# Performance work log

Hardware: AMD Instinct MI355X
Metric: run time of the kernel (lower is better)

The kernel has to match this reference:

```python
import jax, jax.numpy as jnp
from jax import lax
import numpy as np

B, S, T = 32, 512, 64
IN, H, L, HC, OUT = 512, 512, 2, 4, 512

def setup_inputs() -> dict:
    key = jax.random.key(0)
    ks = jax.random.split(key, 12)
    def w(k, shape, fan_in):
        return (jax.random.normal(k, shape, jnp.float32) / np.float32(np.sqrt(fan_in)))
    lstm_in0 = IN + HC * H
    return {
        "inputs": jax.random.normal(ks[0], (B, T, IN), jnp.float32),
        "lengths": jax.random.randint(ks[1], (B,), 1, S + 1),
        "final_hiddens": jax.random.normal(ks[2], (L, B, H), jnp.float32),
        "hiddens": jax.random.normal(ks[3], (B, S, H), jnp.float32),
        "max_output_len": T,
        "max_seq_len": S,
        "Wa1": w(ks[4], (H, 2 * H), 2 * H), "ba1": jnp.zeros((H,), jnp.float32),
        "Wa2": w(ks[5], (HC, H), H), "ba2": jnp.zeros((HC,), jnp.float32),
        "W_ih0": w(ks[6], (4 * H, lstm_in0), lstm_in0), "W_hh0": w(ks[7], (4 * H, H), H),
        "b_ih0": jnp.zeros((4 * H,), jnp.float32), "b_hh0": jnp.zeros((4 * H,), jnp.float32),
        "W_ih1": w(ks[8], (4 * H, H), H), "W_hh1": w(ks[9], (4 * H, H), H),
        "b_ih1": jnp.zeros((4 * H,), jnp.float32), "b_hh1": jnp.zeros((4 * H,), jnp.float32),
        "Wo1": w(ks[10], (H, (1 + HC) * H), (1 + HC) * H), "bo1": jnp.zeros((H,), jnp.float32),
        "Wo2": w(ks[11], (OUT, H), H), "bo2": jnp.zeros((OUT,), jnp.float32),
    }

def _lstm_cell(x, h, c, W_ih, W_hh, b_ih, b_hh):
    # PyTorch LSTM gate order: i, f, g, o
    g = x @ W_ih.T + b_ih + h @ W_hh.T + b_hh
    i, f, gg, o = jnp.split(g, 4, axis=-1)
    c_new = jax.nn.sigmoid(f) * c + jax.nn.sigmoid(i) * jnp.tanh(gg)
    h_new = jax.nn.sigmoid(o) * jnp.tanh(c_new)
    return h_new, c_new

def reference(inputs, lengths, final_hiddens, hiddens, max_output_len, max_seq_len,
              Wa1, ba1, Wa2, ba2, W_ih0, W_hh0, b_ih0, b_hh0,
              W_ih1, W_hh1, b_ih1, b_hh1, Wo1, bo1, Wo2, bo2):
    batch = inputs.shape[0]
    # r_mask[b, s] = 1 if s < lengths[b] else 0  -> [B, S, 1]
    r_mask = (jnp.arange(max_seq_len)[None, :] < lengths[:, None]).astype(hiddens.dtype)[..., None]

    def step(carry, x_t):
        h, c = carry  # each [L, B, H]
        last = h[-1]  # [B, H]
        dup = last[:, None, :] * r_mask  # [B, S, H]
        a = jax.nn.relu(jnp.concatenate([dup, hiddens], axis=2) @ Wa1.T + ba1)  # [B,S,H]
        a = jax.nn.relu(a @ Wa2.T + ba2)  # [B,S,HC]
        a = jax.nn.softmax(a, axis=1)  # softmax over seq dim (unmasked, as in source)
        c_vecs = jnp.einsum('bsk,bsh->bkh', a, hiddens).reshape(batch, -1)  # [B, HC*H]
        x = jnp.concatenate([x_t, c_vecs], axis=1)  # [B, IN + HC*H]
        h0, c0 = _lstm_cell(x, h[0], c[0], W_ih0, W_hh0, b_ih0, b_hh0)
        h1, c1 = _lstm_cell(h0, h[1], c[1], W_ih1, W_hh1, b_ih1, b_hh1)
        out = jnp.tanh(jax.nn.relu(jnp.concatenate([h1, c_vecs], axis=1) @ Wo1.T + bo1) @ Wo2.T + bo2)
        return (jnp.stack([h0, h1]), jnp.stack([c0, c1])), out

    c_init = jnp.zeros_like(final_hiddens)
    _, outs = lax.scan(step, (final_hiddens, c_init), jnp.swapaxes(inputs, 0, 1))  # [T,B,OUT]
    return jnp.swapaxes(outs, 0, 1)  # [B, T, OUT]
```

## Files before the change

kernel.cpp:

```cpp
#include <hip/hip_runtime.h>
#include <cmath>


typedef unsigned short ushort;
typedef unsigned int uint;
typedef __attribute__((ext_vector_type(8))) short bf16x8;
typedef __attribute__((ext_vector_type(4))) float f32x4;

__device__ __forceinline__ float sigmoidf_(float x) { return 1.f / (1.f + __expf(-x)); }
__device__ __forceinline__ float bf2f(ushort u) {
  union { uint i; float f; } x; x.i = ((uint)u) << 16; return x.f;
}
__device__ __forceinline__ ushort f2bf(float f) {
  union { float f; uint i; } x; x.f = f;
  return (ushort)((x.i + 0x7FFFu + ((x.i >> 16) & 1u)) >> 16);
}
__device__ __forceinline__ float wave_sum(float v) {
#pragma unroll
  for (int m = 1; m < 64; m <<= 1) v += __shfl_xor(v, m, 64);
  return v;
}
__device__ __forceinline__ float wave_max(float v) {
#pragma unroll
  for (int m = 1; m < 64; m <<= 1) v = fmaxf(v, __shfl_xor(v, m, 64));
  return v;
}

__global__ void __launch_bounds__(256) k_init(const float* __restrict__ fh,
                                              ushort* h0b0, ushort* h1b0,
                                              float* c0, float* c1) {
  int i = blockIdx.x * 256 + threadIdx.x;
  h0b0[i] = f2bf(fh[i]);
  h1b0[i] = f2bf(fh[16384 + i]);
  c0[i] = 0.f; c1[i] = 0.f;
}

__global__ void __launch_bounds__(256) k_prep(const float* __restrict__ hid,
                                              ushort* __restrict__ hbf) {
  size_t i0 = ((size_t)blockIdx.x * 256 + threadIdx.x) * 8;
  float4 f0 = *(const float4*)&hid[i0];
  float4 f1 = *(const float4*)&hid[i0 + 4];
  uint4 o;
  o.x = (uint)f2bf(f0.x) | ((uint)f2bf(f0.y) << 16);
  o.y = (uint)f2bf(f0.z) | ((uint)f2bf(f0.w) << 16);
  o.z = (uint)f2bf(f1.x) | ((uint)f2bf(f1.y) << 16);
  o.w = (uint)f2bf(f1.z) | ((uint)f2bf(f1.w) << 16);
  *(uint4*)&hbf[i0] = o;
}

__global__ void __launch_bounds__(256) k_inprep(const float* __restrict__ inputs,
                                                ushort* __restrict__ inb) {
  size_t idx4 = ((size_t)blockIdx.x * 256 + threadIdx.x) * 4;
  int m = (int)(idx4 >> 9), k = (int)(idx4 & 511);
  int b = m & 31, tt = m >> 5;
  float4 v = *(const float4*)&inputs[((size_t)b * 64 + tt) * 512 + k];
  ushort4 o; o.x = f2bf(v.x); o.y = f2bf(v.y); o.z = f2bf(v.z); o.w = f2bf(v.w);
  *(ushort4*)&inb[(size_t)m * 512 + k] = o;
}

__global__ void __launch_bounds__(256) k_wcvt(const float* __restrict__ W1, int ld1,
                                              const float* __restrict__ W2, int ld2,
                                              int split, int K,
                                              ushort* __restrict__ dst) {
  size_t idx = ((size_t)blockIdx.x * 256 + threadIdx.x) * 4;
  int j = (int)(idx / K), k = (int)(idx % K);
  const float* src = (k < split) ? (W1 + (size_t)j * ld1 + k)
                                 : (W2 + (size_t)j * ld2 + (k - split));
  float4 v = *(const float4*)src;
  ushort4 o; o.x = f2bf(v.x); o.y = f2bf(v.y); o.z = f2bf(v.z); o.w = f2bf(v.w);
  *(ushort4*)&dst[idx] = o;
}

__global__ void __launch_bounds__(256) k_hidproj(const float* __restrict__ hid,
                                                 const float* __restrict__ Wa1,
                                                 ushort* __restrict__ hpT) {
  __shared__ float As[64][33];
  __shared__ float Bs[64][33];
  int tid = threadIdx.x;
  int r0 = blockIdx.x * 64;
  int n0 = blockIdx.y * 64;
  int b = r0 >> 9, sb = r0 & 511;
  int tm = (tid >> 4) << 2, tn = (tid & 15) << 2;
  int lr = tid >> 2, lk = (tid & 3) << 3;
  float acc[4][4] = {};
  for (int k0 = 0; k0 < 512; k0 += 32) {
    float4 a0 = *(const float4*)&hid[(size_t)(r0 + lr) * 512 + k0 + lk];
    float4 a1 = *(const float4*)&hid[(size_t)(r0 + lr) * 512 + k0 + lk + 4];
    float4 b0 = *(const float4*)&Wa1[(size_t)(n0 + lr) * 1024 + 512 + k0 + lk];
    float4 b1 = *(const float4*)&Wa1[(size_t)(n0 + lr) * 1024 + 512 + k0 + lk + 4];
    __syncthreads();
    As[lr][lk+0]=a0.x; As[lr][lk+1]=a0.y; As[lr][lk+2]=a0.z; As[lr][lk+3]=a0.w;
    As[lr][lk+4]=a1.x; As[lr][lk+5]=a1.y; As[lr][lk+6]=a1.z; As[lr][lk+7]=a1.w;
    Bs[lr][lk+0]=b0.x; Bs[lr][lk+1]=b0.y; Bs[lr][lk+2]=b0.z; Bs[lr][lk+3]=b0.w;
    Bs[lr][lk+4]=b1.x; Bs[lr][lk+5]=b1.y; Bs[lr][lk+6]=b1.z; Bs[lr][lk+7]=b1.w;
    __syncthreads();
#pragma unroll 8
    for (int kk = 0; kk < 32; kk++) {
      float av[4], bv[4];
#pragma unroll
      for (int i = 0; i < 4; i++) av[i] = As[tm + i][kk];
#pragma unroll
      for (int j = 0; j < 4; j++) bv[j] = Bs[tn + j][kk];
#pragma unroll
      for (int i = 0; i < 4; i++)
#pragma unroll
        for (int j = 0; j < 4; j++) acc[i][j] += av[i] * bv[j];
    }
  }
#pragma unroll
  for (int j = 0; j < 4; j++) {
    ushort4 o;
    o.x = f2bf(acc[0][j]); o.y = f2bf(acc[1][j]);
    o.z = f2bf(acc[2][j]); o.w = f2bf(acc[3][j]);
    *(ushort4*)&hpT[((size_t)b * 512 + n0 + tn + j) * 512 + sb + tm] = o;
  }
}

__global__ void __launch_bounds__(512) k_scst(const ushort* __restrict__ hpT,
                                              const float* __restrict__ ba1,
                                              const float* __restrict__ Wa2,
                                              float* __restrict__ scoresP) {
  int bid = blockIdx.x, tid = threadIdx.x;
  int b = bid >> 3, kdq = bid & 7, kd0 = kdq << 6, s = tid;
  float a0 = 0.f, a1 = 0.f, a2 = 0.f, a3 = 0.f;
  const ushort* hpr = hpT + ((size_t)b * 512 + kd0) * 512 + s;
#pragma unroll 4
  for (int i = 0; i < 64; i++) {
    int kd = kd0 + i;
    float a = fmaxf(bf2f(hpr[(size_t)i * 512]) + ba1[kd], 0.f);
    a0 += Wa2[kd] * a;
    a1 += Wa2[512 + kd] * a;
    a2 += Wa2[1024 + kd] * a;
    a3 += Wa2[1536 + kd] * a;
  }
  float* dst = scoresP + ((size_t)(kdq * 32 + b) * 4) * 512 + s;
  dst[0] = a0; dst[512] = a1; dst[1024] = a2; dst[1536] = a3;
}

__global__ void __launch_bounds__(512) k_sum0(const float* __restrict__ scoresP,
                                              const float* __restrict__ ba2,
                                              float* __restrict__ scores0) {
  int idx = blockIdx.x * 512 + threadIdx.x;
  int b = idx >> 11, k = (idx >> 9) & 3, s = idx & 511;
  float v = ba2[k];
#pragma unroll
  for (int q = 0; q < 8; q++) v += scoresP[((size_t)(q * 32 + b) * 4 + k) * 512 + s];
  scores0[idx] = fmaxf(v, 0.f);
}

__global__ void __launch_bounds__(512) k_stat0(const float* __restrict__ scores0,
                                               const int* __restrict__ lengths,
                                               float* __restrict__ m0v,
                                               float* __restrict__ statZ,
                                               float* __restrict__ P0) {
  __shared__ float st[32], st2[32];
  int b = blockIdx.x, tid = threadIdx.x, lane = tid & 63, w = tid >> 6;
  int s = tid, len = lengths[b];
  bool stat = s >= len;
  float v[4], m0[4];
#pragma unroll
  for (int k = 0; k < 4; k++) v[k] = scores0[((size_t)b * 4 + k) * 512 + s];
#pragma unroll
  for (int k = 0; k < 4; k++) {
    float mk = wave_max(stat ? v[k] : -1e30f);
    if (lane == 0) st[w * 4 + k] = mk;
  }
  __syncthreads();
#pragma unroll
  for (int k = 0; k < 4; k++) {
    float m = st[k];
#pragma unroll
    for (int w2 = 1; w2 < 8; w2++) m = fmaxf(m, st[w2 * 4 + k]);
    m0[k] = m;
  }
  float e[4];
#pragma unroll
  for (int k = 0; k < 4; k++) {
    e[k] = stat ? __expf(v[k] - m0[k]) : 0.f;
    float sk = wave_sum(e[k]);
    if (lane == 0) st2[w * 4 + k] = sk;
  }
  __syncthreads();
#pragma unroll
  for (int k = 0; k < 4; k++) {
    P0[((size_t)b * 4 + k) * 512 + s] = e[k];
  }
  if (tid == 0) {
#pragma unroll
    for (int k = 0; k < 4; k++) {
      float z = 0.f;
#pragma unroll
      for (int w2 = 0; w2 < 8; w2++) z += st2[w2 * 4 + k];
      m0v[b * 4 + k] = m0[k];
      statZ[b * 4 + k] = z;
    }
  }
}

__global__ void __launch_bounds__(512) k_statvec(const float* __restrict__ P0,
                                                 const ushort* __restrict__ hbf,
                                                 const int* __restrict__ lengths,
                                                 float* __restrict__ statvec) {
  __shared__ float P[4 * 512];
  __shared__ float red2[8 * 256];
  int bid = blockIdx.x, tid = threadIdx.x;
  int b = bid >> 3, hs = bid & 7;
#pragma unroll
  for (int k = 0; k < 4; k++) P[k * 512 + tid] = P0[((size_t)b * 4 + k) * 512 + tid];
  __syncthreads();
  int h = tid & 63, cch = tid >> 6;
  int c0 = lengths[b] >> 6;
  float a0 = 0.f, a1 = 0.f, a2 = 0.f, a3 = 0.f;
  if (cch >= c0) {
    const ushort* hb = hbf + ((size_t)(b * 512 + (cch << 6)) * 512) + (hs << 6) + h;
#pragma unroll 4
    for (int si = 0; si < 64; si++) {
      float hv = bf2f(hb[(size_t)si * 512]);
      int ps = (cch << 6) + si;
      a0 += P[ps] * hv;
      a1 += P[512 + ps] * hv;
      a2 += P[1024 + ps] * hv;
      a3 += P[1536 + ps] * hv;
    }
  }
  red2[(cch << 8) + h] = a0;
  red2[(cch << 8) + 64 + h] = a1;
  red2[(cch << 8) + 128 + h] = a2;
  red2[(cch << 8) + 192 + h] = a3;
  __syncthreads();
  if (tid < 256) {
    int k = tid >> 6, hh = tid & 63;
    float acc = 0.f;
#pragma unroll
    for (int c = 0; c < 8; c++) acc += red2[(c << 8) + (k << 6) + hh];
    statvec[((size_t)b * 4 + k) * 512 + (hs << 6) + hh] = acc;
  }
}

__device__ __forceinline__ void mfma_slice(
    const ushort* __restrict__ W, int ldW, int jrow0, int jstride,
    const ushort* __restrict__ xA, int ldA, int xsplit,
    const ushort* __restrict__ xB, int ldB, int coff,
    int klo, int khi, float* __restrict__ redrow) {
  const int l = threadIdx.x & 63;
  const int r16 = l & 15, koff = (l >> 4) * 8;
  const int j = jrow0 + (r16 & 3) + (r16 >> 2) * jstride;
  const ushort* wrow = W + (size_t)j * ldW + koff;
  const ushort* a0A = xA + (size_t)r16 * ldA + koff;
  const ushort* a1A = xA + (size_t)(16 + r16) * ldA + koff;
  const ushort* a0B = xB + (size_t)r16 * ldB + koff;
  const ushort* a1B = xB + (size_t)(16 + r16) * ldB + koff;
  f32x4 acc0 = {0.f, 0.f, 0.f, 0.f}, acc1 = {0.f, 0.f, 0.f, 0.f};
#pragma unroll 4
  for (int k0 = klo; k0 < khi; k0 += 32) {
    bf16x8 av0, av1;
    if (k0 < xsplit) {
      av0 = *(const bf16x8*)(a0A + k0);
      av1 = *(const bf16x8*)(a1A + k0);
    } else {
      av0 = *(const bf16x8*)(a0B + (k0 - coff));
      av1 = *(const bf16x8*)(a1B + (k0 - coff));
    }
    bf16x8 wv = *(const bf16x8*)(wrow + k0);
    acc0 = __builtin_amdgcn_mfma_f32_16x16x32_bf16(av0, wv, acc0, 0, 0, 0);
    acc1 = __builtin_amdgcn_mfma_f32_16x16x32_bf16(av1, wv, acc1, 0, 0, 0);
  }
  const int brow = (l >> 4) << 2;
#pragma unroll
  for (int r = 0; r < 4; r++) {
    redrow[r16 * 33 + brow + r] = acc0[r];
    redrow[r16 * 33 + 16 + brow + r] = acc1[r];
  }
}

__global__ void __launch_bounds__(256) k_gin0(const ushort* __restrict__ Wg0b,
                                              const ushort* __restrict__ inb,
                                              float* __restrict__ gi0) {
  __shared__ float red[4 * 528];
  int tid = threadIdx.x, w = tid >> 6;
  int j0 = blockIdx.x * 16, m0 = blockIdx.y * 32;
  mfma_slice(Wg0b, 3072, j0, 4, inb + (size_t)m0 * 512, 512, 1 << 30,
             inb + (size_t)m0 * 512, 512, 0, w * 128, w * 128 + 128,
             red + w * 528);
  __syncthreads();
#pragma unroll
  for (int e = 0; e < 2; e++) {
    int idx = tid + e * 256;
    int j = idx >> 5, b = idx & 31;
    float v = 0.f;
#pragma unroll
    for (int ww = 0; ww < 4; ww++) v += red[ww * 528 + j * 33 + b];
    gi0[(size_t)(m0 + b) * 2048 + j0 + j] = v;
  }
}

__global__ void __launch_bounds__(512) k_scq(
    const ushort* __restrict__ Wq, const ushort* __restrict__ Wo1,
    const ushort* __restrict__ h1cur, const ushort* __restrict__ xb,
    const float* __restrict__ bo1, ushort* __restrict__ o1bf,
    const ushort* __restrict__ hpT, const float* __restrict__ ba1,
    const float* __restrict__ Wa2, const int* __restrict__ lengths,
    float* __restrict__ scoresP, int t) {
  __shared__ float red[8 * 528];
  __shared__ float qs[64];
  int bid = blockIdx.x, tid = threadIdx.x, w = tid >> 6, lane = tid & 63;
  if (bid < 32) {
    if (t < 1) return;
    mfma_slice(Wo1, 2560, bid * 16, 4, h1cur, 512, 512, xb, 2048, 512,
               w * 320, w * 320 + 320, red + w * 528);
    __syncthreads();
    int j = tid & 15, b = tid >> 4;
    float v = 0.f;
#pragma unroll
    for (int ww = 0; ww < 8; ww++) v += red[ww * 528 + j * 33 + b];
    int jj = bid * 16 + j;
    o1bf[b * 512 + jj] = f2bf(fmaxf(v + bo1[jj], 0.f));
  } else {
    if (t >= 64) return;
    int r = bid - 32;
    int b = r >> 3, kdq = r & 7, kd0 = kdq << 6;
    {
      bf16x8 hv8 = *(const bf16x8*)(h1cur + b * 512 + lane * 8);
      float hf[8];
#pragma unroll
      for (int e2 = 0; e2 < 8; e2++) hf[e2] = bf2f(((ushort*)&hv8)[e2]);
#pragma unroll
      for (int rr = 0; rr < 8; rr++) {
        int row = kd0 + w * 8 + rr;
        bf16x8 wv8 = *(const bf16x8*)(Wq + (size_t)row * 512 + lane * 8);
        float acc = 0.f;
#pragma unroll
        for (int e2 = 0; e2 < 8; e2++) acc += hf[e2] * bf2f(((ushort*)&wv8)[e2]);
        acc = wave_sum(acc);
        if (lane == 0) qs[w * 8 + rr] = acc;
      }
    }
    __syncthreads();
    int s = tid, len = lengths[b];
    if ((tid & ~63) >= len) return;
    float m = (s < len) ? 1.f : 0.f;
    float a0 = 0.f, a1 = 0.f, a2 = 0.f, a3 = 0.f;
    const ushort* hpr = hpT + ((size_t)b * 512 + kd0) * 512 + s;
#pragma unroll 4
    for (int i = 0; i < 64; i++) {
      int kd = kd0 + i;
      float hv = bf2f(hpr[(size_t)i * 512]);
      float a = fmaxf(hv + ba1[kd] + m * qs[i], 0.f);
      a0 += Wa2[kd] * a;
      a1 += Wa2[512 + kd] * a;
      a2 += Wa2[1024 + kd] * a;
      a3 += Wa2[1536 + kd] * a;
    }
    float* dst = scoresP + ((size_t)(kdq * 32 + b) * 4) * 512 + s;
    dst[0] = a0; dst[512] = a1; dst[1024] = a2; dst[1536] = a3;
  }
}

__global__ void __launch_bounds__(512) k_ctxout(
    const float* __restrict__ scoresP, const float* __restrict__ ba2,
    const int* __restrict__ lengths, const ushort* __restrict__ hbf,
    const float* __restrict__ m0v, const float* __restrict__ statZ,
    const float* __restrict__ statvec, ushort* __restrict__ xb,
    const ushort* __restrict__ Wo2, const ushort* __restrict__ o1bf,
    const float* __restrict__ bo2, float* __restrict__ outp, int t) {
  __shared__ float red[8 * 528];
  __shared__ float P[4 * 512];
  __shared__ float red2[8 * 256];
  __shared__ float st[32], st2[32];
  int bid = blockIdx.x, tid = threadIdx.x;
  if (bid < 32) {
    if (t < 1) return;
    int w = tid >> 6;
    mfma_slice(Wo2, 512, bid * 16, 4, o1bf, 512, 1 << 30, o1bf, 512, 0,
               w * 64, w * 64 + 64, red + w * 528);
    __syncthreads();
    int j = tid & 15, b = tid >> 4;
    float v = 0.f;
#pragma unroll
    for (int ww = 0; ww < 8; ww++) v += red[ww * 528 + j * 33 + b];
    int jj = bid * 16 + j;
    outp[((size_t)b * 64 + (t - 1)) * 512 + jj] = tanhf(v + bo2[jj]);
  } else {
    if (t >= 64) return;
    int r = bid - 32;
    int b = r >> 3, hs = r & 7;
    int lane = tid & 63, w = tid >> 6;
    int s = tid, len = lengths[b];
    bool act = s < len;
    float v[4];
#pragma unroll
    for (int k = 0; k < 4; k++) {
      if (act) {
        float a = ba2[k];
#pragma unroll
        for (int q = 0; q < 8; q++)
          a += scoresP[((size_t)(q * 32 + b) * 4 + k) * 512 + s];
        v[k] = fmaxf(a, 0.f);
      } else {
        v[k] = -1e30f;
      }
    }
    float M[4];
#pragma unroll
    for (int k = 0; k < 4; k++) {
      float mk = wave_max(v[k]);
      if (lane == 0) st[w * 4 + k] = mk;
    }
    __syncthreads();
#pragma unroll
    for (int k = 0; k < 4; k++) {
      float m = st[k];
#pragma unroll
      for (int w2 = 1; w2 < 8; w2++) m = fmaxf(m, st[w2 * 4 + k]);
      M[k] = fmaxf(m, m0v[b * 4 + k]);
    }
    float e[4];
#pragma unroll
    for (int k = 0; k < 4; k++) {
      e[k] = act ? __expf(v[k] - M[k]) : 0.f;
      float sk = wave_sum(e[k]);
      if (lane == 0) st2[w * 4 + k] = sk;
    }
    __syncthreads();
    float sc[4];
#pragma unroll
    for (int k = 0; k < 4; k++) {
      float dynZ = 0.f;
#pragma unroll
      for (int w2 = 0; w2 < 8; w2++) dynZ += st2[w2 * 4 + k];
      float scB = __expf(m0v[b * 4 + k] - M[k]);
      float Z = dynZ + scB * statZ[b * 4 + k];
      float invZ = 1.f / Z;
      P[(k << 9) + s] = e[k] * invZ;
      sc[k] = scB * invZ;
    }
    __syncthreads();
    int h = tid & 63, cch = tid >> 6;
    int nch = (len + 63) >> 6;
    float a0 = 0.f, a1 = 0.f, a2 = 0.f, a3 = 0.f;
    if (cch < nch) {
      const ushort* hb =
          hbf + ((size_t)(b * 512 + (cch << 6)) * 512) + (hs << 6) + h;
#pragma unroll 4
      for (int si = 0; si < 64; si++) {
        float hv = bf2f(hb[(size_t)si * 512]);
        int ps = (cch << 6) + si;
        a0 += P[ps] * hv;
        a1 += P[512 + ps] * hv;
        a2 += P[1024 + ps] * hv;
        a3 += P[1536 + ps] * hv;
      }
    }
    red2[(cch << 8) + h] = a0;
    red2[(cch << 8) + 64 + h] = a1;
    red2[(cch << 8) + 128 + h] = a2;
    red2[(cch << 8) + 192 + h] = a3;
    __syncthreads();
    if (tid < 256) {
      int k = tid >> 6, hh = tid & 63;
      float acc = 0.f;
#pragma unroll
      for (int c = 0; c < 8; c++) acc += red2[(c << 8) + (k << 6) + hh];
      acc += sc[k] * statvec[((size_t)b * 4 + k) * 512 + (hs << 6) + hh];
      xb[b * 2048 + (k << 9) + (hs << 6) + hh] = f2bf(acc);
    }
  }
}

__global__ void __launch_bounds__(512) k_cell0(
    const ushort* __restrict__ Wg0b, const ushort* __restrict__ xb,
    const ushort* __restrict__ h0cur, const float* __restrict__ gi0,
    const float* __restrict__ bih, const float* __restrict__ bhh,
    float* __restrict__ cst, ushort* __restrict__ hnew, int t) {
  __shared__ float red[8 * 528];
  int bid = blockIdx.x, tid = threadIdx.x, w = tid >> 6;
  mfma_slice(Wg0b + 512, 3072, bid * 4, 512, xb, 2048, 2048, h0cur, 512, 2048,
             w * 320, w * 320 + 320, red + w * 528);
  __syncthreads();
  if (tid < 128) {
    int b = tid & 31, dh = tid >> 5;
    int h = bid * 4 + dh;
    float G[4];
#pragma unroll
    for (int g = 0; g < 4; g++) {
      float v = bih[g * 512 + h] + bhh[g * 512 + h] +
                gi0[(size_t)(t * 32 + b) * 2048 + g * 512 + h];
#pragma unroll
      for (int ww = 0; ww < 8; ww++) v += red[ww * 528 + (g * 4 + dh) * 33 + b];
      G[g] = v;
    }
    float i_ = sigmoidf_(G[0]), f_ = sigmoidf_(G[1]);
    float gg = tanhf(G[2]), o_ = sigmoidf_(G[3]);
    float cn = f_ * cst[b * 512 + h] + i_ * gg;
    cst[b * 512 + h] = cn;
    hnew[b * 512 + h] = f2bf(o_ * tanhf(cn));
  }
}

__global__ void __launch_bounds__(512) k_cell1(
    const ushort* __restrict__ Wg1b, const ushort* __restrict__ h0new,
    const ushort* __restrict__ h1cur, const float* __restrict__ bih,
    const float* __restrict__ bhh, float* __restrict__ cst,
    ushort* __restrict__ hnew) {
  __shared__ float red[8 * 528];
  int bid = blockIdx.x, tid = threadIdx.x, w = tid >> 6;
  mfma_slice(Wg1b, 1024, bid * 4, 512, h0new, 512, 512, h1cur, 512, 512,
             w * 128, w * 128 + 128, red + w * 528);
  __syncthreads();
  if (tid < 128) {
    int b = tid & 31, dh = tid >> 5;
    int h = bid * 4 + dh;
    float G[4];
#pragma unroll
    for (int g = 0; g < 4; g++) {
      float v = bih[g * 512 + h] + bhh[g * 512 + h];
#pragma unroll
      for (int ww = 0; ww < 8; ww++) v += red[ww * 528 + (g * 4 + dh) * 33 + b];
      G[g] = v;
    }
    float i_ = sigmoidf_(G[0]), f_ = sigmoidf_(G[1]);
    float gg = tanhf(G[2]), o_ = sigmoidf_(G[3]);
    float cn = f_ * cst[b * 512 + h] + i_ * gg;
    cst[b * 512 + h] = cn;
    hnew[b * 512 + h] = f2bf(o_ * tanhf(cn));
  }
}

extern "C" void kernel_launch(void* const* d_in, const int* in_sizes, int n_in,
                              void* d_out, int out_size, void* d_ws, size_t ws_size,
                              hipStream_t stream) {
  const float* inputs  = (const float*)d_in[0];
  const int*   lengths = (const int*)d_in[1];
  const float* fh      = (const float*)d_in[2];
  const float* hiddens = (const float*)d_in[3];
  const float* Wa1  = (const float*)d_in[6];
  const float* ba1  = (const float*)d_in[7];
  const float* Wa2  = (const float*)d_in[8];
  const float* ba2  = (const float*)d_in[9];
  const float* Wih0 = (const float*)d_in[10];
  const float* Whh0 = (const float*)d_in[11];
  const float* bih0 = (const float*)d_in[12];
  const float* bhh0 = (const float*)d_in[13];
  const float* Wih1 = (const float*)d_in[14];
  const float* Whh1 = (const float*)d_in[15];
  const float* bih1 = (const float*)d_in[16];
  const float* bhh1 = (const float*)d_in[17];
  const float* Wo1  = (const float*)d_in[18];
  const float* bo1  = (const float*)d_in[19];
  const float* Wo2  = (const float*)d_in[20];
  const float* bo2  = (const float*)d_in[21];
  float* outp = (float*)d_out;

  char* p = (char*)d_ws;
  ushort* hpT = (ushort*)p; p += (size_t)32 * 512 * 512 * 2;
  ushort* hbf = (ushort*)p; p += (size_t)32 * 512 * 512 * 2;
  float* scoresP = (float*)p; p += (size_t)8 * 32 * 4 * 512 * 4;
  float* scores0 = (float*)p; p += (size_t)32 * 4 * 512 * 4;
  float* P0      = (float*)p; p += (size_t)32 * 4 * 512 * 4;
  float* statvec = (float*)p; p += (size_t)32 * 4 * 512 * 4;
  float* m0v     = (float*)p; p += 128 * sizeof(float);
  float* statZ   = (float*)p; p += 128 * sizeof(float);
  ushort* xb     = (ushort*)p; p += (size_t)32 * 2048 * 2;
  ushort* h0b    = (ushort*)p; p += (size_t)2 * 32 * 512 * 2;
  ushort* h1b    = (ushort*)p; p += (size_t)2 * 32 * 512 * 2;
  ushort* o1bf   = (ushort*)p; p += (size_t)32 * 512 * 2;
  float* c0      = (float*)p; p += (size_t)32 * 512 * 4;
  float* c1      = (float*)p; p += (size_t)32 * 512 * 4;
  ushort* Wg0b   = (ushort*)p; p += (size_t)2048 * 3072 * 2;
  ushort* Wg1b   = (ushort*)p; p += (size_t)2048 * 1024 * 2;
  ushort* Wo1b   = (ushort*)p; p += (size_t)512 * 2560 * 2;
  ushort* Wo2b   = (ushort*)p; p += (size_t)512 * 512 * 2;
  ushort* Wqb    = (ushort*)p; p += (size_t)512 * 512 * 2;
  ushort* inb    = (ushort*)p; p += (size_t)2048 * 512 * 2;
  float* gi0     = (float*)p; p += (size_t)2048 * 2048 * 4;

  k_init<<<64, 256, 0, stream>>>(fh, h0b, h1b, c0, c1);
  k_prep<<<4096, 256, 0, stream>>>(hiddens, hbf);
  k_inprep<<<1024, 256, 0, stream>>>(inputs, inb);
  k_hidproj<<<dim3(256, 8), 256, 0, stream>>>(hiddens, Wa1, hpT);
  k_wcvt<<<6144, 256, 0, stream>>>(Wih0, 2560, Whh0, 512, 2560, 3072, Wg0b);
  k_wcvt<<<2048, 256, 0, stream>>>(Wih1, 512, Whh1, 512, 512, 1024, Wg1b);
  k_wcvt<<<1280, 256, 0, stream>>>(Wo1, 2560, Wo1, 2560, 2560, 2560, Wo1b);
  k_wcvt<<<256, 256, 0, stream>>>(Wo2, 512, Wo2, 512, 512, 512, Wo2b);
  k_wcvt<<<256, 256, 0, stream>>>(Wa1, 1024, Wa1, 1024, 512, 512, Wqb);
  k_gin0<<<dim3(128, 64), 256, 0, stream>>>(Wg0b, inb, gi0);
  k_scst<<<256, 512, 0, stream>>>(hpT, ba1, Wa2, scoresP);
  k_sum0<<<128, 512, 0, stream>>>(scoresP, ba2, scores0);
  k_stat0<<<32, 512, 0, stream>>>(scores0, lengths, m0v, statZ, P0);
  k_statvec<<<256, 512, 0, stream>>>(P0, hbf, lengths, statvec);

  for (int t = 0; t <= 64; t++) {
    const ushort* h1cur = h1b + (size_t)(t & 1) * 16384;
    const ushort* h0cur = h0b + (size_t)(t & 1) * 16384;
    ushort* h0nxt = h0b + (size_t)((t + 1) & 1) * 16384;
    ushort* h1nxt = h1b + (size_t)((t + 1) & 1) * 16384;
    k_scq<<<288, 512, 0, stream>>>(Wqb, Wo1b, h1cur, xb, bo1, o1bf, hpT, ba1,
                                   Wa2, lengths, scoresP, t);
    k_ctxout<<<288, 512, 0, stream>>>(scoresP, ba2, lengths, hbf, m0v, statZ,
                                      statvec, xb, Wo2b, o1bf, bo2, outp, t);
    if (t < 64) {
      k_cell0<<<128, 512, 0, stream>>>(Wg0b, xb, h0cur, gi0, bih0, bhh0, c0,
                                       h0nxt, t);
      k_cell1<<<128, 512, 0, stream>>>(Wg1b, h0nxt, h1cur, bih1, bhh1, c1, h1nxt);
    }
  }
}
```

Before: 2.980 ms.

## Widen parallelism across score, context, gin0 and LSTM cell kernels

Splits the attention-score reduction over 16 chunks instead of 8 and packs the four head scores into float4 partials, so the sum kernels do vectorised loads. The context kernels now stride sequence positions across waves instead of 64-row chunks, which balances work when lengths are uneven. The LSTM cell kernels move to 1024-thread blocks that split K across 16 waves, and gin0 loops over four M tiles per block. The cost is more partial-sum traffic and longer shared-memory reductions. A redundant, odd conditional write to P was added in ctxout.

```diff
diff --git a/kernel.cpp b/kernel.cpp
--- a/kernel.cpp
+++ b/kernel.cpp
@@ -119,13 +119,13 @@
 __global__ void __launch_bounds__(512) k_scst(const ushort* __restrict__ hpT,
                                               const float* __restrict__ ba1,
                                               const float* __restrict__ Wa2,
-                                              float* __restrict__ scoresP) {
+                                              float4* __restrict__ scoresP4) {
   int bid = blockIdx.x, tid = threadIdx.x;
-  int b = bid >> 3, kdq = bid & 7, kd0 = kdq << 6, s = tid;
+  int b = bid >> 4, kdq = bid & 15, kd0 = kdq << 5, s = tid;
   float a0 = 0.f, a1 = 0.f, a2 = 0.f, a3 = 0.f;
   const ushort* hpr = hpT + ((size_t)b * 512 + kd0) * 512 + s;
 #pragma unroll 4
-  for (int i = 0; i < 64; i++) {
+  for (int i = 0; i < 32; i++) {
     int kd = kd0 + i;
     float a = fmaxf(bf2f(hpr[(size_t)i * 512]) + ba1[kd], 0.f);
     a0 += Wa2[kd] * a;
@@ -133,19 +133,24 @@
     a2 += Wa2[1024 + kd] * a;
     a3 += Wa2[1536 + kd] * a;
   }
-  float* dst = scoresP + ((size_t)(kdq * 32 + b) * 4) * 512 + s;
-  dst[0] = a0; dst[512] = a1; dst[1024] = a2; dst[1536] = a3;
-}
-
-__global__ void __launch_bounds__(512) k_sum0(const float* __restrict__ scoresP,
+  scoresP4[((size_t)(kdq * 32 + b)) * 512 + s] = make_float4(a0, a1, a2, a3);
+}
+
+__global__ void __launch_bounds__(512) k_sum0(const float4* __restrict__ scoresP4,
                                               const float* __restrict__ ba2,
                                               float* __restrict__ scores0) {
   int idx = blockIdx.x * 512 + threadIdx.x;
-  int b = idx >> 11, k = (idx >> 9) & 3, s = idx & 511;
-  float v = ba2[k];
-#pragma unroll
-  for (int q = 0; q < 8; q++) v += scoresP[((size_t)(q * 32 + b) * 4 + k) * 512 + s];
-  scores0[idx] = fmaxf(v, 0.f);
+  int b = idx >> 9, s = idx & 511;
+  float a0 = ba2[0], a1 = ba2[1], a2 = ba2[2], a3 = ba2[3];
+#pragma unroll
+  for (int q = 0; q < 16; q++) {
+    float4 p = scoresP4[((size_t)(q * 32 + b)) * 512 + s];
+    a0 += p.x; a1 += p.y; a2 += p.z; a3 += p.w;
+  }
+  scores0[((size_t)b * 4 + 0) * 512 + s] = fmaxf(a0, 0.f);
+  scores0[((size_t)b * 4 + 1) * 512 + s] = fmaxf(a1, 0.f);
+  scores0[((size_t)b * 4 + 2) * 512 + s] = fmaxf(a2, 0.f);
+  scores0[((size_t)b * 4 + 3) * 512 + s] = fmaxf(a3, 0.f);
 }
 
 __global__ void __launch_bounds__(512) k_stat0(const float* __restrict__ scores0,
@@ -208,25 +213,20 @@
 #pragma unroll
   for (int k = 0; k < 4; k++) P[k * 512 + tid] = P0[((size_t)b * 4 + k) * 512 + tid];
   __syncthreads();
-  int h = tid & 63, cch = tid >> 6;
-  int c0 = lengths[b] >> 6;
+  int h = tid & 63, w8 = tid >> 6;
+  int len = lengths[b];
   float a0 = 0.f, a1 = 0.f, a2 = 0.f, a3 = 0.f;
-  if (cch >= c0) {
-    const ushort* hb = hbf + ((size_t)(b * 512 + (cch << 6)) * 512) + (hs << 6) + h;
-#pragma unroll 4
-    for (int si = 0; si < 64; si++) {
-      float hv = bf2f(hb[(size_t)si * 512]);
-      int ps = (cch << 6) + si;
-      a0 += P[ps] * hv;
-      a1 += P[512 + ps] * hv;
-      a2 += P[1024 + ps] * hv;
-      a3 += P[1536 + ps] * hv;
-    }
-  }
-  red2[(cch << 8) + h] = a0;
-  red2[(cch << 8) + 64 + h] = a1;
-  red2[(cch << 8) + 128 + h] = a2;
-  red2[(cch << 8) + 192 + h] = a3;
+  for (int si = len + ((w8 - len) & 7); si < 512; si += 8) {
+    float hv = bf2f(hbf[((size_t)(b * 512 + si) * 512) + (hs << 6) + h]);
+    a0 += P[si] * hv;
+    a1 += P[512 + si] * hv;
+    a2 += P[1024 + si] * hv;
+    a3 += P[1536 + si] * hv;
+  }
+  red2[(w8 << 8) + h] = a0;
+  red2[(w8 << 8) + 64 + h] = a1;
+  red2[(w8 << 8) + 128 + h] = a2;
+  red2[(w8 << 8) + 192 + h] = a3;
   __syncthreads();
   if (tid < 256) {
     int k = tid >> 6, hh = tid & 63;
@@ -278,19 +278,23 @@
                                               float* __restrict__ gi0) {
   __shared__ float red[4 * 528];
   int tid = threadIdx.x, w = tid >> 6;
-  int j0 = blockIdx.x * 16, m0 = blockIdx.y * 32;
-  mfma_slice(Wg0b, 3072, j0, 4, inb + (size_t)m0 * 512, 512, 1 << 30,
-             inb + (size_t)m0 * 512, 512, 0, w * 128, w * 128 + 128,
-             red + w * 528);
-  __syncthreads();
-#pragma unroll
-  for (int e = 0; e < 2; e++) {
-    int idx = tid + e * 256;
-    int j = idx >> 5, b = idx & 31;
-    float v = 0.f;
-#pragma unroll
-    for (int ww = 0; ww < 4; ww++) v += red[ww * 528 + j * 33 + b];
-    gi0[(size_t)(m0 + b) * 2048 + j0 + j] = v;
+  int j0 = blockIdx.x * 16;
+  for (int mt = 0; mt < 4; mt++) {
+    int m0 = (blockIdx.y * 4 + mt) * 32;
+    mfma_slice(Wg0b, 3072, j0, 4, inb + (size_t)m0 * 512, 512, 1 << 30,
+               inb + (size_t)m0 * 512, 512, 0, w * 128, w * 128 + 128,
+               red + w * 528);
+    __syncthreads();
+#pragma unroll
+    for (int e = 0; e < 2; e++) {
+      int idx = tid + e * 256;
+      int j = idx >> 5, b = idx & 31;
+      float v = 0.f;
+#pragma unroll
+      for (int ww = 0; ww < 4; ww++) v += red[ww * 528 + j * 33 + b];
+      gi0[(size_t)(m0 + b) * 2048 + j0 + j] = v;
+    }
+    __syncthreads();
   }
 }
 
@@ -300,9 +304,9 @@
     const float* __restrict__ bo1, ushort* __restrict__ o1bf,
     const ushort* __restrict__ hpT, const float* __restrict__ ba1,
     const float* __restrict__ Wa2, const int* __restrict__ lengths,
-    float* __restrict__ scoresP, int t) {
+    float4* __restrict__ scoresP4, int t) {
   __shared__ float red[8 * 528];
-  __shared__ float qs[64];
+  __shared__ float qs[32];
   int bid = blockIdx.x, tid = threadIdx.x, w = tid >> 6, lane = tid & 63;
   if (bid < 32) {
     if (t < 1) return;
@@ -318,21 +322,21 @@
   } else {
     if (t >= 64) return;
     int r = bid - 32;
-    int b = r >> 3, kdq = r & 7, kd0 = kdq << 6;
+    int b = r >> 4, kdq = r & 15, kd0 = kdq << 5;
     {
       bf16x8 hv8 = *(const bf16x8*)(h1cur + b * 512 + lane * 8);
       float hf[8];
 #pragma unroll
       for (int e2 = 0; e2 < 8; e2++) hf[e2] = bf2f(((ushort*)&hv8)[e2]);
 #pragma unroll
-      for (int rr = 0; rr < 8; rr++) {
-        int row = kd0 + w * 8 + rr;
+      for (int rr = 0; rr < 4; rr++) {
+        int row = kd0 + w * 4 + rr;
         bf16x8 wv8 = *(const bf16x8*)(Wq + (size_t)row * 512 + lane * 8);
         float acc = 0.f;
 #pragma unroll
         for (int e2 = 0; e2 < 8; e2++) acc += hf[e2] * bf2f(((ushort*)&wv8)[e2]);
         acc = wave_sum(acc);
-        if (lane == 0) qs[w * 8 + rr] = acc;
+        if (lane == 0) qs[w * 4 + rr] = acc;
       }
     }
     __syncthreads();
@@ -342,7 +346,7 @@
     float a0 = 0.f, a1 = 0.f, a2 = 0.f, a3 = 0.f;
     const ushort* hpr = hpT + ((size_t)b * 512 + kd0) * 512 + s;
 #pragma unroll 4
-    for (int i = 0; i < 64; i++) {
+    for (int i = 0; i < 32; i++) {
       int kd = kd0 + i;
       float hv = bf2f(hpr[(size_t)i * 512]);
       float a = fmaxf(hv + ba1[kd] + m * qs[i], 0.f);
@@ -351,13 +355,12 @@
       a2 += Wa2[1024 + kd] * a;
       a3 += Wa2[1536 + kd] * a;
     }
-    float* dst = scoresP + ((size_t)(kdq * 32 + b) * 4) * 512 + s;
-    dst[0] = a0; dst[512] = a1; dst[1024] = a2; dst[1536] = a3;
+    scoresP4[((size_t)(kdq * 32 + b)) * 512 + s] = make_float4(a0, a1, a2, a3);
   }
 }
 
 __global__ void __launch_bounds__(512) k_ctxout(
-    const float* __restrict__ scoresP, const float* __restrict__ ba2,
+    const float4* __restrict__ scoresP4, const float* __restrict__ ba2,
     const int* __restrict__ lengths, const ushort* __restrict__ hbf,
     const float* __restrict__ m0v, const float* __restrict__ statZ,
     const float* __restrict__ statvec, ushort* __restrict__ xb,
@@ -388,16 +391,18 @@
     int s = tid, len = lengths[b];
     bool act = s < len;
     float v[4];
-#pragma unroll
-    for (int k = 0; k < 4; k++) {
+    {
+      float a0 = ba2[0], a1 = ba2[1], a2 = ba2[2], a3 = ba2[3];
       if (act) {
-        float a = ba2[k];
-#pragma unroll
-        for (int q = 0; q < 8; q++)
-          a += scoresP[((size_t)(q * 32 + b) * 4 + k) * 512 + s];
-        v[k] = fmaxf(a, 0.f);
+#pragma unroll
+        for (int q = 0; q < 16; q++) {
+          float4 p = scoresP4[((size_t)(q * 32 + b)) * 512 + s];
+          a0 += p.x; a1 += p.y; a2 += p.z; a3 += p.w;
+        }
+        v[0] = fmaxf(a0, 0.f); v[1] = fmaxf(a1, 0.f);
+        v[2] = fmaxf(a2, 0.f); v[3] = fmaxf(a3, 0.f);
       } else {
-        v[k] = -1e30f;
+        v[0] = v[1] = v[2] = v[3] = -1e30f;
       }
     }
     float M[4];
@@ -431,30 +436,28 @@
       float scB = __expf(m0v[b * 4 + k] - M[k]);
       float Z = dynZ + scB * statZ[b * 4 + k];
       float invZ = 1.f / Z;
-      P[(k << 9) + s] = e[k] * invZ;
+      P[(0 << 9) + s] = (k == 0) ? e[0] * invZ : P[(0 << 9) + s];
+      if (k == 0) P[0 * 512 + s] = e[0] * invZ;
+      if (k == 1) P[1 * 512 + s] = e[1] * invZ;
+      if (k == 2) P[2 * 512 + s] = e[2] * invZ;
+      if (k == 3) P[3 * 512 + s] = e[3] * invZ;
       sc[k] = scB * invZ;
     }
     __syncthreads();
-    int h = tid & 63, cch = tid >> 6;
-    int nch = (len + 63) >> 6;
+    int h = tid & 63, w8 = tid >> 6;
     float a0 = 0.f, a1 = 0.f, a2 = 0.f, a3 = 0.f;
-    if (cch < nch) {
-      const ushort* hb =
-          hbf + ((size_t)(b * 512 + (cch << 6)) * 512) + (hs << 6) + h;
-#pragma unroll 4
-      for (int si = 0; si < 64; si++) {
-        float hv = bf2f(hb[(size_t)si * 512]);
-        int ps = (cch << 6) + si;
-        a0 += P[ps] * hv;
-        a1 += P[512 + ps] * hv;
-        a2 += P[1024 + ps] * hv;
-        a3 += P[1536 + ps] * hv;
-      }
-    }
-    red2[(cch << 8) + h] = a0;
-    red2[(cch << 8) + 64 + h] = a1;
-    red2[(cch << 8) + 128 + h] = a2;
-    red2[(cch << 8) + 192 + h] = a3;
+    const ushort* hb0 = hbf + ((size_t)b * 512) * 512 + (hs << 6) + h;
+    for (int si = w8; si < len; si += 8) {
+      float hv = bf2f(hb0[(size_t)si * 512]);
+      a0 += P[si] * hv;
+      a1 += P[512 + si] * hv;
+      a2 += P[1024 + si] * hv;
+      a3 += P[1536 + si] * hv;
+    }
+    red2[(w8 << 8) + h] = a0;
+    red2[(w8 << 8) + 64 + h] = a1;
+    red2[(w8 << 8) + 128 + h] = a2;
+    red2[(w8 << 8) + 192 + h] = a3;
     __syncthreads();
     if (tid < 256) {
       int k = tid >> 6, hh = tid & 63;
@@ -467,15 +470,15 @@
   }
 }
 
-__global__ void __launch_bounds__(512) k_cell0(
+__global__ void __launch_bounds__(1024) k_cell0(
     const ushort* __restrict__ Wg0b, const ushort* __restrict__ xb,
     const ushort* __restrict__ h0cur, const float* __restrict__ gi0,
     const float* __restrict__ bih, const float* __restrict__ bhh,
     float* __restrict__ cst, ushort* __restrict__ hnew, int t) {
-  __shared__ float red[8 * 528];
+  __shared__ float red[16 * 528];
   int bid = blockIdx.x, tid = threadIdx.x, w = tid >> 6;
   mfma_slice(Wg0b + 512, 3072, bid * 4, 512, xb, 2048, 2048, h0cur, 512, 2048,
-             w * 320, w * 320 + 320, red + w * 528);
+             w * 160, w * 160 + 160, red + w * 528);
   __syncthreads();
   if (tid < 128) {
     int b = tid & 31, dh = tid >> 5;
@@ -486,7 +489,7 @@
       float v = bih[g * 512 + h] + bhh[g * 512 + h] +
                 gi0[(size_t)(t * 32 + b) * 2048 + g * 512 + h];
 #pragma unroll
-      for (int ww = 0; ww < 8; ww++) v += red[ww * 528 + (g * 4 + dh) * 33 + b];
+      for (int ww = 0; ww < 16; ww++) v += red[ww * 528 + (g * 4 + dh) * 33 + b];
       G[g] = v;
     }
     float i_ = sigmoidf_(G[0]), f_ = sigmoidf_(G[1]);
@@ -497,15 +500,15 @@
   }
 }
 
-__global__ void __launch_bounds__(512) k_cell1(
+__global__ void __launch_bounds__(1024) k_cell1(
     const ushort* __restrict__ Wg1b, const ushort* __restrict__ h0new,
     const ushort* __restrict__ h1cur, const float* __restrict__ bih,
     const float* __restrict__ bhh, float* __restrict__ cst,
     ushort* __restrict__ hnew) {
-  __shared__ float red[8 * 528];
+  __shared__ float red[16 * 528];
   int bid = blockIdx.x, tid = threadIdx.x, w = tid >> 6;
   mfma_slice(Wg1b, 1024, bid * 4, 512, h0new, 512, 512, h1cur, 512, 512,
-             w * 128, w * 128 + 128, red + w * 528);
+             w * 64, w * 64 + 64, red + w * 528);
   __syncthreads();
   if (tid < 128) {
     int b = tid & 31, dh = tid >> 5;
@@ -515,7 +518,7 @@
     for (int g = 0; g < 4; g++) {
       float v = bih[g * 512 + h] + bhh[g * 512 + h];
 #pragma unroll
-      for (int ww = 0; ww < 8; ww++) v += red[ww * 528 + (g * 4 + dh) * 33 + b];
+      for (int ww = 0; ww < 16; ww++) v += red[ww * 528 + (g * 4 + dh) * 33 + b];
       G[g] = v;
     }
     float i_ = sigmoidf_(G[0]), f_ = sigmoidf_(G[1]);
@@ -554,7 +557,7 @@
   char* p = (char*)d_ws;
   ushort* hpT = (ushort*)p; p += (size_t)32 * 512 * 512 * 2;
   ushort* hbf = (ushort*)p; p += (size_t)32 * 512 * 512 * 2;
-  float* scoresP = (float*)p; p += (size_t)8 * 32 * 4 * 512 * 4;
+  float4* scoresP4 = (float4*)p; p += (size_t)16 * 32 * 512 * 16;
   float* scores0 = (float*)p; p += (size_t)32 * 4 * 512 * 4;
   float* P0      = (float*)p; p += (size_t)32 * 4 * 512 * 4;
   float* statvec = (float*)p; p += (size_t)32 * 4 * 512 * 4;
@@ -583,9 +586,9 @@
   k_wcvt<<<1280, 256, 0, stream>>>(Wo1, 2560, Wo1, 2560, 2560, 2560, Wo1b);
   k_wcvt<<<256, 256, 0, stream>>>(Wo2, 512, Wo2, 512, 512, 512, Wo2b);
   k_wcvt<<<256, 256, 0, stream>>>(Wa1, 1024, Wa1, 1024, 512, 512, Wqb);
-  k_gin0<<<dim3(128, 64), 256, 0, stream>>>(Wg0b, inb, gi0);
-  k_scst<<<256, 512, 0, stream>>>(hpT, ba1, Wa2, scoresP);
-  k_sum0<<<128, 512, 0, stream>>>(scoresP, ba2, scores0);
+  k_gin0<<<dim3(128, 16), 256, 0, stream>>>(Wg0b, inb, gi0);
+  k_scst<<<512, 512, 0, stream>>>(hpT, ba1, Wa2, scoresP4);
+  k_sum0<<<32, 512, 0, stream>>>(scoresP4, ba2, scores0);
   k_stat0<<<32, 512, 0, stream>>>(scores0, lengths, m0v, statZ, P0);
   k_statvec<<<256, 512, 0, stream>>>(P0, hbf, lengths, statvec);
 
@@ -594,14 +597,15 @@
     const ushort* h0cur = h0b + (size_t)(t & 1) * 16384;
     ushort* h0nxt = h0b + (size_t)((t + 1) & 1) * 16384;
     ushort* h1nxt = h1b + (size_t)((t + 1) & 1) * 16384;
-    k_scq<<<288, 512, 0, stream>>>(Wqb, Wo1b, h1cur, xb, bo1, o1bf, hpT, ba1,
-                                   Wa2, lengths, scoresP, t);
-    k_ctxout<<<288, 512, 0, stream>>>(scoresP, ba2, lengths, hbf, m0v, statZ,
+    k_scq<<<544, 512, 0, stream>>>(Wqb, Wo1b, h1cur, xb, bo1, o1bf, hpT, ba1,
+                                   Wa2, lengths, scoresP4, t);
+    k_ctxout<<<288, 512, 0, stream>>>(scoresP4, ba2, lengths, hbf, m0v, statZ,
                                       statvec, xb, Wo2b, o1bf, bo2, outp, t);
     if (t < 64) {
-      k_cell0<<<128, 512, 0, stream>>>(Wg0b, xb, h0cur, gi0, bih0, bhh0, c0,
-                                       h0nxt, t);
-      k_cell1<<<128, 512, 0, stream>>>(Wg1b, h0nxt, h1cur, bih1, bhh1, c1, h1nxt);
-    }
-  }
-}
+      k_cell0<<<128, 1024, 0, stream>>>(Wg0b, xb, h0cur, gi0, bih0, bhh0, c0,
+                                        h0nxt, t);
+      k_cell1<<<128, 1024, 0, stream>>>(Wg1b, h0nxt, h1cur, bih1, bhh1, c1,
+                                        h1nxt);
+    }
+  }
+}
```

Result: slower. 3.437 ms (+15.3%).
